# Kernel tuning notes

Hardware: AMD Instinct MI355X
Metric: run time of the kernel (lower is better)

The kernel has to match this reference:

```python
import jax, jax.numpy as jnp
import numpy as np

NUM_HEADS = 8
CHUNK = 2
TAU = 2.0

# --- LIF neuron with ATan surrogate gradient (spikingjelly MultiStepLIFNode, hard reset to 0, detach_reset) ---
@jax.custom_vjp
def spike(x):
    return (x >= 0.0).astype(x.dtype)

def _spike_fwd(x):
    return spike(x), x

def _spike_bwd(x, g):
    alpha = 2.0
    sg = (alpha / 2.0) / (1.0 + (jnp.pi / 2.0 * alpha * x) ** 2)
    return (g * sg,)

spike.defvjp(_spike_fwd, _spike_bwd)

def lif(x_seq, v_th=1.0):
    # x_seq: [T, ...]; v' = v + (x - v)/tau ; spike if v' >= v_th ; hard reset v=0 (reset path detached)
    def step(v, x):
        v = v + (x - v) / TAU
        s = spike(v - v_th)
        v = v * (1.0 - jax.lax.stop_gradient(s))
        return v, s
    _, s = jax.lax.scan(step, jnp.zeros_like(x_seq[0]), x_seq)
    return s

def conv1x1_bn(x, W, scale, bias, conv_bias=None):
    # 1x1 conv over channel dim + eval-mode BN (per-channel affine)
    y = jnp.einsum('tbchw,dc->tbdhw', x, W)
    if conv_bias is not None:
        y = y + conv_bias[None, None, :, None, None]
    return y * scale[None, None, :, None, None] + bias[None, None, :, None, None]


def setup_inputs() -> dict:
    key = jax.random.key(0)
    ks = jax.random.split(key, 16)
    T, B, C, H, W = 4, 32, 512, 16, 16
    s = 1.0 / np.sqrt(C)
    return {
        'x': jax.random.normal(ks[0], (T, B, C, H, W), jnp.float32),
        'Wq': jax.random.normal(ks[1], (C, C), jnp.float32) * s,
        'q_scale': jax.random.uniform(ks[2], (C,), jnp.float32, 0.5, 1.5),
        'q_bias': jax.random.normal(ks[3], (C,), jnp.float32) * 0.1,
        'Wk': jax.random.normal(ks[4], (C, C), jnp.float32) * s,
        'k_scale': jax.random.uniform(ks[5], (C,), jnp.float32, 0.5, 1.5),
        'k_bias': jax.random.normal(ks[6], (C,), jnp.float32) * 0.1,
        'Wv': jax.random.normal(ks[7], (C, C), jnp.float32) * s,
        'v_scale': jax.random.uniform(ks[8], (C,), jnp.float32, 0.5, 1.5),
        'v_bias': jax.random.normal(ks[9], (C,), jnp.float32) * 0.1,
        'Wp': jax.random.normal(ks[10], (C, C), jnp.float32) * s,
        'bp': jax.random.normal(ks[11], (C,), jnp.float32) * 0.1,
        'p_scale': jax.random.uniform(ks[12], (C,), jnp.float32, 0.5, 1.5),
        'p_bias': jax.random.normal(ks[13], (C,), jnp.float32) * 0.1,
    }


def reference(x, Wq, q_scale, q_bias, Wk, k_scale, k_bias, Wv, v_scale, v_bias, Wp, bp, p_scale, p_bias):
    T, B, C, H, W = x.shape
    N = H * W
    hd = C // NUM_HEADS
    identity = x

    xs = lif(x)  # shortcut_lif

    def qkv_branch(W_, sc, bi):
        y = lif(conv1x1_bn(xs, W_, sc, bi))           # [T,B,C,H,W] spikes
        # flatten(3).transpose(-1,-2).reshape(...heads...).permute == split C, swap N/hd
        return jnp.swapaxes(y.reshape(T, B, NUM_HEADS, hd, N), -1, -2)  # [T,B,h,N,hd]

    q = qkv_branch(Wq, q_scale, q_bias)
    k = qkv_branch(Wk, k_scale, k_bias)
    v = qkv_branch(Wv, v_scale, v_bias)

    # STAtten: temporal chunking, linear attention q @ (k^T v)
    scaling = 1.0 / H
    nc = T // CHUNK

    def to_chunks(y):  # [T,B,h,N,hd] -> [nc,B,h,CHUNK*N,hd]
        return (y.reshape(nc, CHUNK, B, NUM_HEADS, N, hd)
                 .transpose(0, 2, 3, 1, 4, 5)
                 .reshape(nc, B, NUM_HEADS, CHUNK * N, hd))

    qc, kc, vc = to_chunks(q), to_chunks(k), to_chunks(v)
    attn = jnp.einsum('nbhsd,nbhse->nbhde', kc, vc) * scaling   # [nc,B,h,hd,hd]
    out = jnp.einsum('nbhsd,nbhde->nbhse', qc, attn)            # [nc,B,h,CHUNK*N,hd]
    out = (out.reshape(nc, B, NUM_HEADS, CHUNK, N, hd)
              .transpose(0, 3, 1, 2, 4, 5)
              .reshape(T, B, NUM_HEADS, N, hd))

    x2 = jnp.swapaxes(out, -1, -2).reshape(T, B, C, N)          # [T,B,C,N]
    x2 = lif(x2, v_th=0.5).reshape(T, B, C, H, W)               # attn_lif

    x3 = conv1x1_bn(x2, Wp, p_scale, p_bias, conv_bias=bp)      # proj conv+BN
    return x3 + identity, v
```

## Files before the change

### kernel.cpp

```cpp
#include <hip/hip_runtime.h>

typedef unsigned short ushort_t;
typedef unsigned char u8;
typedef short bf16x8 __attribute__((ext_vector_type(8)));
typedef float f32x4 __attribute__((ext_vector_type(4)));

#define T_DIM 4
#define B_DIM 32
#define C_DIM 512
#define N_DIM 256

__device__ __forceinline__ float bf2f(ushort_t u) {
  union { unsigned int i; float f; } x;
  x.i = ((unsigned int)u) << 16;
  return x.f;
}
__device__ __forceinline__ ushort_t f2bf(float f) {
  unsigned int u = __float_as_uint(f);
  u = (u + 0x7FFFu + ((u >> 16) & 1u)) >> 16;
  return (ushort_t)u;
}

__device__ __forceinline__ void gload16(const void* g, void* l) {
  __builtin_amdgcn_global_load_lds(
      (const __attribute__((address_space(1))) unsigned int*)g,
      (__attribute__((address_space(3))) unsigned int*)l, 16, 0, 0);
}

__global__ __launch_bounds__(256) void k0_split(
    const float* __restrict__ Wq, const float* __restrict__ Wk,
    const float* __restrict__ Wv, const float* __restrict__ Wp,
    ushort_t* __restrict__ Sqkv, ushort_t* __restrict__ Sp)
{
  int gid = blockIdx.x * 256 + threadIdx.x;
  int w = gid >> 15;
  int off = (gid & 32767) * 8;
  const float* src = (w == 0) ? Wq : ((w == 1) ? Wk : ((w == 2) ? Wv : Wp));
  ushort_t* dst = (w < 3) ? (Sqkv + (size_t)w * 3 * 262144) : Sp;
  float wv[8];
  *(float4*)&wv[0] = *(const float4*)(src + off);
  *(float4*)&wv[4] = *(const float4*)(src + off + 4);
  ushort_t hi[8], mi[8], lo[8];
#pragma unroll
  for (int i = 0; i < 8; i++) {
    float f = wv[i];
    ushort_t h = f2bf(f);  float r  = f - bf2f(h);
    ushort_t m = f2bf(r);  float r2 = r - bf2f(m);
    ushort_t l = f2bf(r2);
    hi[i] = h; mi[i] = m; lo[i] = l;
  }
  *(uint4*)(dst + off)              = *(uint4*)&hi[0];
  *(uint4*)(dst + 262144 + off)     = *(uint4*)&mi[0];
  *(uint4*)(dst + 2 * 262144 + off) = *(uint4*)&lo[0];
}

__global__ __launch_bounds__(256) void k1_shortcut_lif(
    const float* __restrict__ x, u8* __restrict__ xsT8)
{
  const int n0 = blockIdx.x * 64;
  const int c0 = blockIdx.y * 64;
  const int b  = blockIdx.z;
  __shared__ u8 sm[64][80];
  const int tid = threadIdx.x;
  const int r  = tid >> 2;
  const int j0 = (tid & 3) * 16;
  float v[16];
#pragma unroll
  for (int i = 0; i < 16; i++) v[i] = 0.f;
  for (int t = 0; t < T_DIM; t++) {
    const float* xp = x + ((((size_t)t * B_DIM + b) * C_DIM) + c0 + r) * N_DIM + n0 + j0;
    float xv[16];
    *(float4*)&xv[0]  = *(const float4*)xp;
    *(float4*)&xv[4]  = *(const float4*)(xp + 4);
    *(float4*)&xv[8]  = *(const float4*)(xp + 8);
    *(float4*)&xv[12] = *(const float4*)(xp + 12);
    __syncthreads();
#pragma unroll
    for (int i = 0; i < 16; i++) {
      float nv = v[i] + (xv[i] - v[i]) * 0.5f;
      bool s = (nv >= 1.0f);
      v[i] = s ? 0.f : nv;
      sm[j0 + i][r] = s ? (u8)1 : (u8)0;
    }
    __syncthreads();
    union { uint4 u; u8 b[16]; } ov;
#pragma unroll
    for (int i = 0; i < 16; i++) ov.b[i] = sm[r][j0 + i];
    u8* op = xsT8 + ((((size_t)t * B_DIM + b) * N_DIM) + n0 + r) * C_DIM + c0 + j0;
    *(uint4*)op = ov.u;
  }
}

__global__ __launch_bounds__(512, 4) void k2_qkv(
    const u8* __restrict__ xsT8, const ushort_t* __restrict__ Sqkv,
    const float* __restrict__ qsc, const float* __restrict__ qbi,
    const float* __restrict__ ksc, const float* __restrict__ kbi,
    const float* __restrict__ vsc, const float* __restrict__ vbi,
    u8* __restrict__ qs8, u8* __restrict__ ks8, float* __restrict__ vout,
    u8* __restrict__ vs8)
{
  const int lin = blockIdx.x + blockIdx.y * 24;
  const int b   = (lin & 7) | (((lin >> 3) & 3) << 3);
  const int mt  = lin >> 5;
  const int branch = mt >> 3;
  const int mloc = (mt & 7) * 64;
  const ushort_t* Ws = Sqkv + (size_t)branch * 3 * 262144;
  const float* scp = (branch == 0) ? qsc : ((branch == 1) ? ksc : vsc);
  const float* bip = (branch == 0) ? qbi : ((branch == 1) ? kbi : vbi);

  __shared__ alignas(16) ushort_t As[4][2][64][32];
  __shared__ alignas(16) u8 Bs8[4][256][32];

  const int tid  = threadIdx.x;
  const int lane = tid & 63;
  const int wave = tid >> 6;
  const int wrow = (wave >> 1) * 16;
  const int wcol = (wave & 1) * 128;
  const int frow = lane & 15;
  const int fsl  = lane >> 4;

  const u8* Bb0 = xsT8 + (size_t)b * N_DIM * C_DIM;

  const int a0p = wave >> 2, a0q = wave & 3;
  const int arl = lane >> 2;
  const int acl = (((lane & 3) ^ ((arl >> 1) & 3)) * 8);
  const int brl = lane >> 1;
  const int bcl = (((lane & 1) ^ ((brl >> 2) & 1) ^ ((brl >> 3) & 1)) * 16);
  const int cbx = wave;

#define K2_STAGE(s_) {                                                                     \
    const int ss_ = (s_);                                                                  \
    const int t_ = ss_ >> 4; const int kb_ = (ss_ & 15) * 32; const int bf_ = ss_ & 3;     \
    gload16(Ws + (size_t)a0p * 262144 + (size_t)(mloc + a0q * 16 + arl) * 512 + kb_ + acl, \
            &As[bf_][a0p][a0q * 16][0]);                                                   \
    gload16(Bb0 + (size_t)t_ * (B_DIM * N_DIM * C_DIM) + (size_t)(cbx * 32 + brl) * 512 + kb_ + bcl, \
            &Bs8[bf_][cbx * 32][0]);                                                       \
  }

  f32x4 acc[8];
  float vst[32];
#pragma unroll
  for (int i = 0; i < 32; i++) vst[i] = 0.f;
#pragma unroll
  for (int j = 0; j < 8; j++) acc[j] = (f32x4){0.f, 0.f, 0.f, 0.f};

  const int crow0 = (lane >> 4) * 4;
  const int cn    = lane & 15;
  float sc4[4], bi4[4];
#pragma unroll
  for (int r = 0; r < 4; r++) {
    int c = mloc + wrow + crow0 + r;
    sc4[r] = scp[c]; bi4[r] = bip[c];
  }

  K2_STAGE(0);
  K2_STAGE(1);

  for (int s = 0; s < 64; s++) {
    const int cur = s & 3;
    if (s < 62) K2_STAGE(s + 2);

    if (s < 62)      asm volatile("s_waitcnt vmcnt(4)" ::: "memory");
    else if (s == 62) asm volatile("s_waitcnt vmcnt(2)" ::: "memory");
    else              asm volatile("s_waitcnt vmcnt(0)" ::: "memory");
    __builtin_amdgcn_s_barrier();
    __builtin_amdgcn_sched_barrier(0);

    bf16x8 af[2];
    const int ar = wrow + frow;
    const int asw = (fsl ^ ((ar >> 1) & 3)) * 8;
#pragma unroll
    for (int p = 0; p < 2; p++) af[p] = *(const bf16x8*)&As[cur][p][ar][asw];

#pragma unroll
    for (int j = 0; j < 8; j++) {
      const int row = wcol + j * 16 + frow;
      const int bx  = ((row >> 2) ^ (row >> 3)) & 1;
      const int bsw = (((fsl >> 1) ^ bx) << 4) + ((fsl & 1) << 3);
      uint2 raw = *(const uint2*)&Bs8[cur][row][bsw];
      union { bf16x8 v; unsigned int u[4]; } bu;
      bu.u[0] = __builtin_amdgcn_perm(0u, raw.x, 0x05010400u) * 0x3F80u;
      bu.u[1] = __builtin_amdgcn_perm(0u, raw.x, 0x07030602u) * 0x3F80u;
      bu.u[2] = __builtin_amdgcn_perm(0u, raw.y, 0x05010400u) * 0x3F80u;
      bu.u[3] = __builtin_amdgcn_perm(0u, raw.y, 0x07030602u) * 0x3F80u;
#pragma unroll
      for (int p = 0; p < 2; p++)
        acc[j] = __builtin_amdgcn_mfma_f32_16x16x32_bf16(af[p], bu.v, acc[j], 0, 0, 0);
    }

    if ((s & 15) == 15) {
      const int t = s >> 4;
      const size_t tb = (size_t)t * B_DIM + b;
      if (branch < 2) {
        u8* dst = (branch == 0) ? qs8 : ks8;
#pragma unroll
        for (int r = 0; r < 4; r++) {
          const int c = mloc + wrow + crow0 + r;
#pragma unroll
          for (int j = 0; j < 8; j++) {
            const int n = wcol + j * 16 + cn;
            float y = acc[j][r] * sc4[r] + bi4[r];
            const int vi = j * 4 + r;
            float v = vst[vi];
            v = v + (y - v) * 0.5f;
            bool sp = (v >= 1.0f);
            vst[vi] = sp ? 0.f : v;
            dst[(tb * C_DIM + c) * N_DIM + n] = sp ? (u8)1 : (u8)0;
          }
        }
      } else {
        const int hv = mloc >> 6;
        const int d0 = wrow + crow0;
#pragma unroll
        for (int j = 0; j < 8; j++) {
          const int n = wcol + j * 16 + cn;
          float ov[4];
          u8 sv[4];
#pragma unroll
          for (int r = 0; r < 4; r++) {
            float y = acc[j][r] * sc4[r] + bi4[r];
            const int vi = j * 4 + r;
            float v = vst[vi];
            v = v + (y - v) * 0.5f;
            bool sp = (v >= 1.0f);
            vst[vi] = sp ? 0.f : v;
            ov[r] = sp ? 1.0f : 0.0f;
            sv[r] = sp ? (u8)1 : (u8)0;
          }
          const size_t vbase = ((tb * 8 + hv) * N_DIM + n) * 64 + d0;
          *(float4*)(vout + vbase) = make_float4(ov[0], ov[1], ov[2], ov[3]);
          *(uchar4*)(vs8 + vbase)  = make_uchar4(sv[0], sv[1], sv[2], sv[3]);
        }
      }
#pragma unroll
      for (int j = 0; j < 8; j++) acc[j] = (f32x4){0.f, 0.f, 0.f, 0.f};
    }
  }
#undef K2_STAGE
}

__global__ __launch_bounds__(256) void k3_attn(
    const u8* __restrict__ ks8, const u8* __restrict__ vs8,
    float* __restrict__ attn)
{
  const int h  = blockIdx.x;
  const int b  = blockIdx.y;
  const int ch = blockIdx.z;
  __shared__ u8 KtT[64][80];
  __shared__ u8 Vt[64][80];
  const int tid = threadIdx.x;
  const int d0 = (tid >> 4) * 4;
  const int e0 = (tid & 15) * 4;
  float a[16];
#pragma unroll
  for (int i = 0; i < 16; i++) a[i] = 0.f;

  for (int tt = 0; tt < 2; tt++) {
    int t = ch * 2 + tt;
    for (int n0 = 0; n0 < 256; n0 += 64) {
      __syncthreads();
      {
        int d  = tid >> 2;
        int s0 = (tid & 3) * 16;
        union { uint4 u; u8 bvec[16]; } kb;
        kb.u = *(const uint4*)(ks8 + ((((size_t)t * B_DIM + b) * C_DIM) + h * 64 + d) * N_DIM + n0 + s0);
#pragma unroll
        for (int i = 0; i < 16; i++) KtT[s0 + i][d] = kb.bvec[i];
      }
      {
        const u8* vb = vs8 + ((((size_t)t * B_DIM + b) * 8 + h) * N_DIM + n0) * 64;
        int row = tid >> 2;
        int eo  = (tid & 3) * 16;
        *(uint4*)&Vt[row][eo] = *(const uint4*)(vb + (size_t)row * 64 + eo);
      }
      __syncthreads();
      for (int s = 0; s < 64; s++) {
        uchar4 kb = *(const uchar4*)&KtT[s][d0];
        float kv[4] = { (float)kb.x, (float)kb.y, (float)kb.z, (float)kb.w };
        uchar4 vr = *(const uchar4*)&Vt[s][e0];
        float vv[4] = { (float)vr.x, (float)vr.y, (float)vr.z, (float)vr.w };
#pragma unroll
        for (int i = 0; i < 4; i++)
#pragma unroll
          for (int j = 0; j < 4; j++) a[i * 4 + j] += kv[i] * vv[j];
      }
    }
  }
  float* ap = attn + ((((size_t)ch * B_DIM + b) * 8 + h) * 64 + d0) * 64 + e0;
#pragma unroll
  for (int i = 0; i < 4; i++)
#pragma unroll
    for (int j = 0; j < 4; j++)
      ap[i * 64 + j] = a[i * 4 + j] * 0.0625f;
}

__global__ __launch_bounds__(256) void k4_out_lif(
    const u8* __restrict__ qs8, const float* __restrict__ attn,
    u8* __restrict__ x2sT8)
{
  const int h  = blockIdx.x;
  const int b  = blockIdx.y;
  const int nc = blockIdx.z;
  __shared__ float At[64][68];
  __shared__ u8 Qt[64][80];
  const int tid = threadIdx.x;
  const int e0 = (tid >> 4) * 4;
  const int n0 = (tid & 15) * 4;
  float vst[16];
#pragma unroll
  for (int i = 0; i < 16; i++) vst[i] = 0.f;

  for (int t = 0; t < T_DIM; t++) {
    if ((t & 1) == 0) {
      __syncthreads();
      const float* ap = attn + ((((size_t)(t >> 1) * B_DIM + b) * 8) + h) * 4096;
      int dr = tid >> 2;
      int co = (tid & 3) * 16;
#pragma unroll
      for (int u = 0; u < 4; u++)
        *(float4*)&At[dr][co + u * 4] = *(const float4*)(ap + dr * 64 + co + u * 4);
    }
    __syncthreads();
    {
      int d  = tid >> 2;
      int so = (tid & 3) * 16;
      *(uint4*)&Qt[d][so] =
        *(const uint4*)(qs8 + ((((size_t)t * B_DIM + b) * C_DIM) + h * 64 + d) * N_DIM + nc * 64 + so);
    }
    __syncthreads();
    float acc[16];
#pragma unroll
    for (int i = 0; i < 16; i++) acc[i] = 0.f;
    for (int d = 0; d < 64; d++) {
      float4 av = *(const float4*)&At[d][e0];
      float avv[4] = { av.x, av.y, av.z, av.w };
      uchar4 qr = *(const uchar4*)&Qt[d][n0];
      float qv[4] = { (float)qr.x, (float)qr.y, (float)qr.z, (float)qr.w };
#pragma unroll
      for (int i = 0; i < 4; i++)
#pragma unroll
        for (int j = 0; j < 4; j++) acc[i * 4 + j] += avv[i] * qv[j];
    }
#pragma unroll
    for (int j = 0; j < 4; j++) {
      u8 sv[4];
#pragma unroll
      for (int i = 0; i < 4; i++) {
        int vi = i * 4 + j;
        float y = acc[i * 4 + j];
        float nv = vst[vi] + (y - vst[vi]) * 0.5f;
        bool s = (nv >= 0.5f);
        vst[vi] = s ? 0.f : nv;
        sv[i] = s ? (u8)1 : (u8)0;
      }
      int n = nc * 64 + n0 + j;
      u8* op = x2sT8 + ((((size_t)t * B_DIM + b) * N_DIM) + n) * C_DIM + h * 64 + e0;
      *(uchar4*)op = make_uchar4(sv[0], sv[1], sv[2], sv[3]);
    }
  }
}

__global__ __launch_bounds__(512, 4) void k5_proj(
    const u8* __restrict__ x2sT8, const ushort_t* __restrict__ Sp,
    const float* __restrict__ bp, const float* __restrict__ psc,
    const float* __restrict__ pbi,
    const float* __restrict__ x, float* __restrict__ out0)
{
  const int tb = blockIdx.x;
  const int mt = blockIdx.y;
  const int mloc = mt * 64;

  __shared__ alignas(16) ushort_t As[4][2][64][32];
  __shared__ alignas(16) u8 Bs8[4][256][32];

  const int tid  = threadIdx.x;
  const int lane = tid & 63;
  const int wave = tid >> 6;
  const int wrow = (wave >> 1) * 16;
  const int wcol = (wave & 1) * 128;
  const int frow = lane & 15;
  const int fsl  = lane >> 4;

  const u8* Bb = x2sT8 + (size_t)tb * N_DIM * C_DIM;

  const int a0p = wave >> 2, a0q = wave & 3;
  const int arl = lane >> 2;
  const int acl = (((lane & 3) ^ ((arl >> 1) & 3)) * 8);
  const int brl = lane >> 1;
  const int bcl = (((lane & 1) ^ ((brl >> 2) & 1) ^ ((brl >> 3) & 1)) * 16);
  const int cbx = wave;

#define K5_STAGE(s_) {                                                                     \
    const int ss_ = (s_); const int kb_ = ss_ * 32; const int bf_ = ss_ & 3;               \
    gload16(Sp + (size_t)a0p * 262144 + (size_t)(mloc + a0q * 16 + arl) * 512 + kb_ + acl, \
            &As[bf_][a0p][a0q * 16][0]);                                                   \
    gload16(Bb + (size_t)(cbx * 32 + brl) * 512 + kb_ + bcl, &Bs8[bf_][cbx * 32][0]);      \
  }

  f32x4 acc[8];
#pragma unroll
  for (int j = 0; j < 8; j++) acc[j] = (f32x4){0.f, 0.f, 0.f, 0.f};

  K5_STAGE(0);
  K5_STAGE(1);

  for (int s = 0; s < 16; s++) {
    const int cur = s & 3;
    if (s < 14) K5_STAGE(s + 2);

    if (s < 14)       asm volatile("s_waitcnt vmcnt(4)" ::: "memory");
    else if (s == 14) asm volatile("s_waitcnt vmcnt(2)" ::: "memory");
    else              asm volatile("s_waitcnt vmcnt(0)" ::: "memory");
    __builtin_amdgcn_s_barrier();
    __builtin_amdgcn_sched_barrier(0);

    bf16x8 af[2];
    const int ar = wrow + frow;
    const int asw = (fsl ^ ((ar >> 1) & 3)) * 8;
#pragma unroll
    for (int p = 0; p < 2; p++) af[p] = *(const bf16x8*)&As[cur][p][ar][asw];

#pragma unroll
    for (int j = 0; j < 8; j++) {
      const int row = wcol + j * 16 + frow;
      const int bx  = ((row >> 2) ^ (row >> 3)) & 1;
      const int bsw = (((fsl >> 1) ^ bx) << 4) + ((fsl & 1) << 3);
      uint2 raw = *(const uint2*)&Bs8[cur][row][bsw];
      union { bf16x8 v; unsigned int u[4]; } bu;
      bu.u[0] = __builtin_amdgcn_perm(0u, raw.x, 0x05010400u) * 0x3F80u;
      bu.u[1] = __builtin_amdgcn_perm(0u, raw.x, 0x07030602u) * 0x3F80u;
      bu.u[2] = __builtin_amdgcn_perm(0u, raw.y, 0x05010400u) * 0x3F80u;
      bu.u[3] = __builtin_amdgcn_perm(0u, raw.y, 0x07030602u) * 0x3F80u;
#pragma unroll
      for (int p = 0; p < 2; p++)
        acc[j] = __builtin_amdgcn_mfma_f32_16x16x32_bf16(af[p], bu.v, acc[j], 0, 0, 0);
    }
  }

  const int crow0 = (lane >> 4) * 4;
  const int cn    = lane & 15;
#pragma unroll
  for (int r = 0; r < 4; r++) {
    const int c = mloc + wrow + crow0 + r;
    const float scf = psc[c];
    const float bif = pbi[c];
    const float bpf = bp[c];
#pragma unroll
    for (int j = 0; j < 8; j++) {
      const int n = wcol + j * 16 + cn;
      const size_t idx = ((size_t)tb * C_DIM + c) * N_DIM + n;
      out0[idx] = (acc[j][r] + bpf) * scf + bif + x[idx];
    }
  }
#undef K5_STAGE
}

extern "C" void kernel_launch(void* const* d_in, const int* in_sizes, int n_in,
                              void* d_out, int out_size, void* d_ws, size_t ws_size,
                              hipStream_t stream) {
  const float* x   = (const float*)d_in[0];
  const float* Wq  = (const float*)d_in[1];
  const float* qsc = (const float*)d_in[2];
  const float* qbi = (const float*)d_in[3];
  const float* Wk  = (const float*)d_in[4];
  const float* ksc = (const float*)d_in[5];
  const float* kbi = (const float*)d_in[6];
  const float* Wv  = (const float*)d_in[7];
  const float* vsc = (const float*)d_in[8];
  const float* vbi = (const float*)d_in[9];
  const float* Wp  = (const float*)d_in[10];
  const float* bp  = (const float*)d_in[11];
  const float* psc = (const float*)d_in[12];
  const float* pbi = (const float*)d_in[13];

  float* out0 = (float*)d_out;
  float* out1 = out0 + 16777216;

  const size_t M16 = 16u * 1024u * 1024u;
  char* o0 = (char*)d_out;
  char* ws = (char*)d_ws;

  u8*       xsT8  = (u8*)(o0);
  u8*       qs8   = (u8*)(o0 + M16);
  u8*       ks8   = (u8*)(o0 + 2 * M16);
  ushort_t* Sqkv  = (ushort_t*)(o0 + 3 * M16);
  u8*       vs8   = (u8*)(o0 + 3 * M16 + 8u * 1024u * 1024u);
  float*    attn  = (float*)(o0);
  u8*       x2sT8 = (u8*)(ws);
  ushort_t* Sp    = (ushort_t*)(ws + M16);

  hipLaunchKernelGGL(k0_split,        dim3(512),        dim3(256), 0, stream,
                     Wq, Wk, Wv, Wp, Sqkv, Sp);
  hipLaunchKernelGGL(k1_shortcut_lif, dim3(4, 8, 32),   dim3(256), 0, stream, x, xsT8);
  hipLaunchKernelGGL(k2_qkv,          dim3(24, 32),     dim3(512), 0, stream,
                     xsT8, Sqkv, qsc, qbi, ksc, kbi, vsc, vbi, qs8, ks8, out1, vs8);
  hipLaunchKernelGGL(k3_attn,         dim3(8, 32, 2),   dim3(256), 0, stream, ks8, vs8, attn);
  hipLaunchKernelGGL(k4_out_lif,      dim3(8, 32, 4),   dim3(256), 0, stream, qs8, attn, x2sT8);
  hipLaunchKernelGGL(k5_proj,         dim3(128, 8),     dim3(512), 0, stream,
                     x2sT8, Sp, bp, psc, pbi, x, out0);
}
```

Measured before the change: 467.4 us.

## Move attention kernels to MFMA with transposed spike layouts and split-bf16 attn

Rewrites k3 (K^T V) and k4 (Q·attn + LIF) to use bf16 MFMA with async global-to-LDS staging, replacing scalar FMA loops. To feed the MFMAs, k2 now writes q and v spikes in transposed layouts. k3 stores attn as a hi/lo bf16 pair so precision stays close to fp32. Buffer placement also moves Sqkv into workspace. The k2 epilogue's v-spike stores become byte-scattered writes, which may cost some write efficiency.

```diff
diff --git a/kernel.cpp b/kernel.cpp
--- a/kernel.cpp
+++ b/kernel.cpp
@@ -25,6 +25,20 @@
   __builtin_amdgcn_global_load_lds(
       (const __attribute__((address_space(1))) unsigned int*)g,
       (__attribute__((address_space(3))) unsigned int*)l, 16, 0, 0);
+}
+
+__device__ __forceinline__ unsigned int spike2bf(unsigned int w) {
+  unsigned int r;
+  asm("v_mul_u32_u24 %0, 0x3f80, %1" : "=v"(r) : "v"(w));
+  return r;
+}
+__device__ __forceinline__ bf16x8 expand_spikes(uint2 raw) {
+  union { bf16x8 v; unsigned int u[4]; } bu;
+  bu.u[0] = spike2bf(__builtin_amdgcn_perm(0u, raw.x, 0x05010400u));
+  bu.u[1] = spike2bf(__builtin_amdgcn_perm(0u, raw.x, 0x07030602u));
+  bu.u[2] = spike2bf(__builtin_amdgcn_perm(0u, raw.y, 0x05010400u));
+  bu.u[3] = spike2bf(__builtin_amdgcn_perm(0u, raw.y, 0x07030602u));
+  return bu.v;
 }
 
 __global__ __launch_bounds__(256) void k0_split(
@@ -96,8 +110,8 @@
     const float* __restrict__ qsc, const float* __restrict__ qbi,
     const float* __restrict__ ksc, const float* __restrict__ kbi,
     const float* __restrict__ vsc, const float* __restrict__ vbi,
-    u8* __restrict__ qs8, u8* __restrict__ ks8, float* __restrict__ vout,
-    u8* __restrict__ vs8)
+    u8* __restrict__ qs8T, u8* __restrict__ ks8, float* __restrict__ vout,
+    u8* __restrict__ vs8T)
 {
   const int lin = blockIdx.x + blockIdx.y * 24;
   const int b   = (lin & 7) | (((lin >> 3) & 3) << 3);
@@ -160,7 +174,7 @@
     const int cur = s & 3;
     if (s < 62) K2_STAGE(s + 2);
 
-    if (s < 62)      asm volatile("s_waitcnt vmcnt(4)" ::: "memory");
+    if (s < 62)       asm volatile("s_waitcnt vmcnt(4)" ::: "memory");
     else if (s == 62) asm volatile("s_waitcnt vmcnt(2)" ::: "memory");
     else              asm volatile("s_waitcnt vmcnt(0)" ::: "memory");
     __builtin_amdgcn_s_barrier();
@@ -177,22 +191,34 @@
       const int row = wcol + j * 16 + frow;
       const int bx  = ((row >> 2) ^ (row >> 3)) & 1;
       const int bsw = (((fsl >> 1) ^ bx) << 4) + ((fsl & 1) << 3);
-      uint2 raw = *(const uint2*)&Bs8[cur][row][bsw];
-      union { bf16x8 v; unsigned int u[4]; } bu;
-      bu.u[0] = __builtin_amdgcn_perm(0u, raw.x, 0x05010400u) * 0x3F80u;
-      bu.u[1] = __builtin_amdgcn_perm(0u, raw.x, 0x07030602u) * 0x3F80u;
-      bu.u[2] = __builtin_amdgcn_perm(0u, raw.y, 0x05010400u) * 0x3F80u;
-      bu.u[3] = __builtin_amdgcn_perm(0u, raw.y, 0x07030602u) * 0x3F80u;
+      bf16x8 bv = expand_spikes(*(const uint2*)&Bs8[cur][row][bsw]);
 #pragma unroll
       for (int p = 0; p < 2; p++)
-        acc[j] = __builtin_amdgcn_mfma_f32_16x16x32_bf16(af[p], bu.v, acc[j], 0, 0, 0);
+        acc[j] = __builtin_amdgcn_mfma_f32_16x16x32_bf16(af[p], bv, acc[j], 0, 0, 0);
     }
 
     if ((s & 15) == 15) {
       const int t = s >> 4;
       const size_t tb = (size_t)t * B_DIM + b;
-      if (branch < 2) {
-        u8* dst = (branch == 0) ? qs8 : ks8;
+      if (branch == 0) {
+#pragma unroll
+        for (int j = 0; j < 8; j++) {
+          const int n = wcol + j * 16 + cn;
+          u8 sv[4];
+#pragma unroll
+          for (int r = 0; r < 4; r++) {
+            float y = acc[j][r] * sc4[r] + bi4[r];
+            const int vi = j * 4 + r;
+            float v = vst[vi];
+            v = v + (y - v) * 0.5f;
+            bool sp = (v >= 1.0f);
+            vst[vi] = sp ? 0.f : v;
+            sv[r] = sp ? (u8)1 : (u8)0;
+          }
+          *(uchar4*)(qs8T + (tb * N_DIM + n) * C_DIM + mloc + wrow + crow0) =
+              make_uchar4(sv[0], sv[1], sv[2], sv[3]);
+        }
+      } else if (branch == 1) {
 #pragma unroll
         for (int r = 0; r < 4; r++) {
           const int c = mloc + wrow + crow0 + r;
@@ -205,7 +231,7 @@
             v = v + (y - v) * 0.5f;
             bool sp = (v >= 1.0f);
             vst[vi] = sp ? 0.f : v;
-            dst[(tb * C_DIM + c) * N_DIM + n] = sp ? (u8)1 : (u8)0;
+            ks8[(tb * C_DIM + c) * N_DIM + n] = sp ? (u8)1 : (u8)0;
           }
         }
       } else {
@@ -227,9 +253,11 @@
             ov[r] = sp ? 1.0f : 0.0f;
             sv[r] = sp ? (u8)1 : (u8)0;
           }
-          const size_t vbase = ((tb * 8 + hv) * N_DIM + n) * 64 + d0;
-          *(float4*)(vout + vbase) = make_float4(ov[0], ov[1], ov[2], ov[3]);
-          *(uchar4*)(vs8 + vbase)  = make_uchar4(sv[0], sv[1], sv[2], sv[3]);
+          *(float4*)(vout + ((tb * 8 + hv) * N_DIM + n) * 64 + d0) =
+              make_float4(ov[0], ov[1], ov[2], ov[3]);
+#pragma unroll
+          for (int r = 0; r < 4; r++)
+            vs8T[((tb * 8 + hv) * 64 + d0 + r) * N_DIM + n] = sv[r];
         }
       }
 #pragma unroll
@@ -240,124 +268,192 @@
 }
 
 __global__ __launch_bounds__(256) void k3_attn(
-    const u8* __restrict__ ks8, const u8* __restrict__ vs8,
-    float* __restrict__ attn)
+    const u8* __restrict__ ks8, const u8* __restrict__ vs8T,
+    ushort_t* __restrict__ attnT2)
 {
   const int h  = blockIdx.x;
   const int b  = blockIdx.y;
   const int ch = blockIdx.z;
-  __shared__ u8 KtT[64][80];
-  __shared__ u8 Vt[64][80];
-  const int tid = threadIdx.x;
-  const int d0 = (tid >> 4) * 4;
-  const int e0 = (tid & 15) * 4;
-  float a[16];
-#pragma unroll
-  for (int i = 0; i < 16; i++) a[i] = 0.f;
-
-  for (int tt = 0; tt < 2; tt++) {
-    int t = ch * 2 + tt;
-    for (int n0 = 0; n0 < 256; n0 += 64) {
-      __syncthreads();
-      {
-        int d  = tid >> 2;
-        int s0 = (tid & 3) * 16;
-        union { uint4 u; u8 bvec[16]; } kb;
-        kb.u = *(const uint4*)(ks8 + ((((size_t)t * B_DIM + b) * C_DIM) + h * 64 + d) * N_DIM + n0 + s0);
-#pragma unroll
-        for (int i = 0; i < 16; i++) KtT[s0 + i][d] = kb.bvec[i];
-      }
-      {
-        const u8* vb = vs8 + ((((size_t)t * B_DIM + b) * 8 + h) * N_DIM + n0) * 64;
-        int row = tid >> 2;
-        int eo  = (tid & 3) * 16;
-        *(uint4*)&Vt[row][eo] = *(const uint4*)(vb + (size_t)row * 64 + eo);
-      }
-      __syncthreads();
-      for (int s = 0; s < 64; s++) {
-        uchar4 kb = *(const uchar4*)&KtT[s][d0];
-        float kv[4] = { (float)kb.x, (float)kb.y, (float)kb.z, (float)kb.w };
-        uchar4 vr = *(const uchar4*)&Vt[s][e0];
-        float vv[4] = { (float)vr.x, (float)vr.y, (float)vr.z, (float)vr.w };
-#pragma unroll
-        for (int i = 0; i < 4; i++)
-#pragma unroll
-          for (int j = 0; j < 4; j++) a[i * 4 + j] += kv[i] * vv[j];
-      }
-    }
-  }
-  float* ap = attn + ((((size_t)ch * B_DIM + b) * 8 + h) * 64 + d0) * 64 + e0;
-#pragma unroll
-  for (int i = 0; i < 4; i++)
-#pragma unroll
-    for (int j = 0; j < 4; j++)
-      ap[i * 64 + j] = a[i * 4 + j] * 0.0625f;
+  __shared__ alignas(16) u8 Ks[4][64][32];
+  __shared__ alignas(16) u8 Vs[4][64][32];
+  const int tid  = threadIdx.x;
+  const int lane = tid & 63;
+  const int wave = tid >> 6;
+  const int wrow = wave * 16;
+  const int frow = lane & 15;
+  const int fsl  = lane >> 4;
+  const int brl  = lane >> 1;
+  const int bcl  = (((lane & 1) ^ ((brl >> 2) & 1) ^ ((brl >> 3) & 1)) * 16);
+
+#define K3_STAGE(s_) {                                                                     \
+    const int ss_ = (s_);                                                                  \
+    const int t_ = ch * 2 + (ss_ >> 3); const int kb_ = (ss_ & 7) * 32; const int bf_ = ss_ & 3; \
+    if (wave < 2)                                                                          \
+      gload16(ks8 + ((((size_t)t_ * B_DIM + b) * C_DIM) + h * 64 + wave * 32 + brl) * N_DIM + kb_ + bcl, \
+              &Ks[bf_][wave * 32][0]);                                                     \
+    else                                                                                   \
+      gload16(vs8T + ((((size_t)t_ * B_DIM + b) * 8 + h) * 64 + (wave - 2) * 32 + brl) * N_DIM + kb_ + bcl, \
+              &Vs[bf_][(wave - 2) * 32][0]);                                               \
+  }
+
+  f32x4 acc[4];
+#pragma unroll
+  for (int i = 0; i < 4; i++) acc[i] = (f32x4){0.f, 0.f, 0.f, 0.f};
+
+  K3_STAGE(0);
+  K3_STAGE(1);
+
+  for (int s = 0; s < 16; s++) {
+    const int cur = s & 3;
+    if (s < 14) K3_STAGE(s + 2);
+
+    if (s < 14)       asm volatile("s_waitcnt vmcnt(2)" ::: "memory");
+    else if (s == 14) asm volatile("s_waitcnt vmcnt(1)" ::: "memory");
+    else              asm volatile("s_waitcnt vmcnt(0)" ::: "memory");
+    __builtin_amdgcn_s_barrier();
+    __builtin_amdgcn_sched_barrier(0);
+
+    const int arow = wrow + frow;
+    const int axx  = ((arow >> 2) ^ (arow >> 3)) & 1;
+    const int asw  = (((fsl >> 1) ^ axx) << 4) + ((fsl & 1) << 3);
+    bf16x8 af = expand_spikes(*(const uint2*)&Ks[cur][arow][asw]);
+
+#pragma unroll
+    for (int nt = 0; nt < 4; nt++) {
+      const int row = nt * 16 + frow;
+      const int bx  = ((row >> 2) ^ (row >> 3)) & 1;
+      const int bsw = (((fsl >> 1) ^ bx) << 4) + ((fsl & 1) << 3);
+      bf16x8 bv = expand_spikes(*(const uint2*)&Vs[cur][row][bsw]);
+      acc[nt] = __builtin_amdgcn_mfma_f32_16x16x32_bf16(af, bv, acc[nt], 0, 0, 0);
+    }
+  }
+
+  const int cn    = lane & 15;
+  const int crow0 = (lane >> 4) * 4;
+  const int d     = wrow + crow0;
+  const int ks2   = d >> 5;
+  const int dl    = d & 31;
+  const size_t blk = ((size_t)(ch * B_DIM + b) * 8 + h);
+#pragma unroll
+  for (int nt = 0; nt < 4; nt++) {
+    const int e = nt * 16 + cn;
+    union { ushort_t sv[4]; uint2 u; } H, M;
+#pragma unroll
+    for (int r = 0; r < 4; r++) {
+      float a = acc[nt][r] * 0.0625f;
+      ushort_t hi = f2bf(a);
+      float m = a - bf2f(hi);
+      H.sv[r] = hi;
+      M.sv[r] = f2bf(m);
+    }
+    *(uint2*)(attnT2 + ((blk * 2 + 0) * 2 + ks2) * 2048 + (size_t)e * 32 + dl) = H.u;
+    *(uint2*)(attnT2 + ((blk * 2 + 1) * 2 + ks2) * 2048 + (size_t)e * 32 + dl) = M.u;
+  }
+#undef K3_STAGE
 }
 
 __global__ __launch_bounds__(256) void k4_out_lif(
-    const u8* __restrict__ qs8, const float* __restrict__ attn,
+    const u8* __restrict__ qs8T, const ushort_t* __restrict__ attnT2,
     u8* __restrict__ x2sT8)
 {
   const int h  = blockIdx.x;
   const int b  = blockIdx.y;
   const int nc = blockIdx.z;
-  __shared__ float At[64][68];
-  __shared__ u8 Qt[64][80];
-  const int tid = threadIdx.x;
-  const int e0 = (tid >> 4) * 4;
-  const int n0 = (tid & 15) * 4;
-  float vst[16];
-#pragma unroll
-  for (int i = 0; i < 16; i++) vst[i] = 0.f;
-
-  for (int t = 0; t < T_DIM; t++) {
-    if ((t & 1) == 0) {
-      __syncthreads();
-      const float* ap = attn + ((((size_t)(t >> 1) * B_DIM + b) * 8) + h) * 4096;
-      int dr = tid >> 2;
-      int co = (tid & 3) * 16;
-#pragma unroll
-      for (int u = 0; u < 4; u++)
-        *(float4*)&At[dr][co + u * 4] = *(const float4*)(ap + dr * 64 + co + u * 4);
-    }
-    __syncthreads();
-    {
-      int d  = tid >> 2;
-      int so = (tid & 3) * 16;
-      *(uint4*)&Qt[d][so] =
-        *(const uint4*)(qs8 + ((((size_t)t * B_DIM + b) * C_DIM) + h * 64 + d) * N_DIM + nc * 64 + so);
-    }
-    __syncthreads();
-    float acc[16];
-#pragma unroll
-    for (int i = 0; i < 16; i++) acc[i] = 0.f;
-    for (int d = 0; d < 64; d++) {
-      float4 av = *(const float4*)&At[d][e0];
-      float avv[4] = { av.x, av.y, av.z, av.w };
-      uchar4 qr = *(const uchar4*)&Qt[d][n0];
-      float qv[4] = { (float)qr.x, (float)qr.y, (float)qr.z, (float)qr.w };
-#pragma unroll
-      for (int i = 0; i < 4; i++)
-#pragma unroll
-        for (int j = 0; j < 4; j++) acc[i * 4 + j] += avv[i] * qv[j];
-    }
-#pragma unroll
-    for (int j = 0; j < 4; j++) {
-      u8 sv[4];
-#pragma unroll
-      for (int i = 0; i < 4; i++) {
-        int vi = i * 4 + j;
-        float y = acc[i * 4 + j];
-        float nv = vst[vi] + (y - vst[vi]) * 0.5f;
-        bool s = (nv >= 0.5f);
-        vst[vi] = s ? 0.f : nv;
-        sv[i] = s ? (u8)1 : (u8)0;
+  __shared__ alignas(16) ushort_t As[2][2][2][64][32];
+  __shared__ alignas(16) u8 Bs[2][128][32];
+  const int tid  = threadIdx.x;
+  const int lane = tid & 63;
+  const int wave = tid >> 6;
+  const int wrow = wave * 16;
+  const int frow = lane & 15;
+  const int fsl  = lane >> 4;
+  const int arl  = lane >> 2;
+  const int acl  = (((lane & 3) ^ ((arl >> 1) & 3)) * 8);
+  const int brl  = lane >> 1;
+  const int bcl  = (((lane & 1) ^ ((brl >> 2) & 1) ^ ((brl >> 3) & 1)) * 16);
+
+#define K4_STAGEB(s_) {                                                                    \
+    const int ss_ = (s_); const int t_ = ss_ >> 1; const int ks_ = ss_ & 1;                \
+    gload16(qs8T + (((size_t)t_ * B_DIM + b) * N_DIM + nc * 128 + wave * 32 + brl) * C_DIM \
+                 + h * 64 + ks_ * 32 + bcl,                                                \
+            &Bs[ss_ & 1][wave * 32][0]);                                                   \
+  }
+
+#pragma unroll
+  for (int i = 0; i < 8; i++) {
+    const int c  = wave * 8 + i;
+    const int chb = c >> 4, c4 = c & 15;
+    const int p = c4 >> 3, ks = (c4 >> 2) & 1, g = c4 & 3;
+    const size_t blk = ((size_t)(chb * B_DIM + b) * 8 + h);
+    gload16(attnT2 + (((blk * 2 + p) * 2 + ks) * 64 + g * 16 + arl) * 32 + acl,
+            &As[chb][p][ks][g * 16][0]);
+  }
+  K4_STAGEB(0);
+  asm volatile("s_waitcnt vmcnt(0)" ::: "memory");
+  __builtin_amdgcn_s_barrier();
+  __builtin_amdgcn_sched_barrier(0);
+
+  f32x4 acc[8];
+  float vst[32];
+#pragma unroll
+  for (int i = 0; i < 32; i++) vst[i] = 0.f;
+
+  const int cn    = lane & 15;
+  const int crow0 = (lane >> 4) * 4;
+
+  for (int sg = 0; sg < 8; sg++) {
+    const int cur = sg & 1;
+    if (sg < 7) K4_STAGEB(sg + 1);
+
+    const int chb = sg >> 2, ks = sg & 1;
+    if (ks == 0) {
+#pragma unroll
+      for (int j = 0; j < 8; j++) acc[j] = (f32x4){0.f, 0.f, 0.f, 0.f};
+    }
+
+    bf16x8 af[2];
+    const int ar = wrow + frow;
+    const int asw = (fsl ^ ((ar >> 1) & 3)) * 8;
+#pragma unroll
+    for (int p = 0; p < 2; p++) af[p] = *(const bf16x8*)&As[chb][p][ks][ar][asw];
+
+#pragma unroll
+    for (int j = 0; j < 8; j++) {
+      const int row = j * 16 + frow;
+      const int bx  = ((row >> 2) ^ (row >> 3)) & 1;
+      const int bsw = (((fsl >> 1) ^ bx) << 4) + ((fsl & 1) << 3);
+      bf16x8 bv = expand_spikes(*(const uint2*)&Bs[cur][row][bsw]);
+#pragma unroll
+      for (int p = 0; p < 2; p++)
+        acc[j] = __builtin_amdgcn_mfma_f32_16x16x32_bf16(af[p], bv, acc[j], 0, 0, 0);
+    }
+
+    if (ks == 1) {
+      const int t = sg >> 1;
+      const size_t tb = (size_t)t * B_DIM + b;
+#pragma unroll
+      for (int j = 0; j < 8; j++) {
+        const int n = nc * 128 + j * 16 + cn;
+        u8 sv[4];
+#pragma unroll
+        for (int r = 0; r < 4; r++) {
+          const int vi = j * 4 + r;
+          float y = acc[j][r];
+          float nv = vst[vi] + (y - vst[vi]) * 0.5f;
+          bool sp = (nv >= 0.5f);
+          vst[vi] = sp ? 0.f : nv;
+          sv[r] = sp ? (u8)1 : (u8)0;
+        }
+        *(uchar4*)(x2sT8 + (tb * N_DIM + n) * C_DIM + h * 64 + wrow + crow0) =
+            make_uchar4(sv[0], sv[1], sv[2], sv[3]);
       }
-      int n = nc * 64 + n0 + j;
-      u8* op = x2sT8 + ((((size_t)t * B_DIM + b) * N_DIM) + n) * C_DIM + h * 64 + e0;
-      *(uchar4*)op = make_uchar4(sv[0], sv[1], sv[2], sv[3]);
-    }
-  }
+    }
+
+    asm volatile("s_waitcnt vmcnt(0)" ::: "memory");
+    __builtin_amdgcn_s_barrier();
+    __builtin_amdgcn_sched_barrier(0);
+  }
+#undef K4_STAGEB
 }
 
 __global__ __launch_bounds__(512, 4) void k5_proj(
@@ -425,15 +521,10 @@
       const int row = wcol + j * 16 + frow;
       const int bx  = ((row >> 2) ^ (row >> 3)) & 1;
       const int bsw = (((fsl >> 1) ^ bx) << 4) + ((fsl & 1) << 3);
-      uint2 raw = *(const uint2*)&Bs8[cur][row][bsw];
-      union { bf16x8 v; unsigned int u[4]; } bu;
-      bu.u[0] = __builtin_amdgcn_perm(0u, raw.x, 0x05010400u) * 0x3F80u;
-      bu.u[1] = __builtin_amdgcn_perm(0u, raw.x, 0x07030602u) * 0x3F80u;
-      bu.u[2] = __builtin_amdgcn_perm(0u, raw.y, 0x05010400u) * 0x3F80u;
-      bu.u[3] = __builtin_amdgcn_perm(0u, raw.y, 0x07030602u) * 0x3F80u;
+      bf16x8 bv = expand_spikes(*(const uint2*)&Bs8[cur][row][bsw]);
 #pragma unroll
       for (int p = 0; p < 2; p++)
-        acc[j] = __builtin_amdgcn_mfma_f32_16x16x32_bf16(af[p], bu.v, acc[j], 0, 0, 0);
+        acc[j] = __builtin_amdgcn_mfma_f32_16x16x32_bf16(af[p], bv, acc[j], 0, 0, 0);
     }
   }
 
@@ -480,22 +571,24 @@
   char* o0 = (char*)d_out;
   char* ws = (char*)d_ws;
 
-  u8*       xsT8  = (u8*)(o0);
-  u8*       qs8   = (u8*)(o0 + M16);
-  u8*       ks8   = (u8*)(o0 + 2 * M16);
-  ushort_t* Sqkv  = (ushort_t*)(o0 + 3 * M16);
-  u8*       vs8   = (u8*)(o0 + 3 * M16 + 8u * 1024u * 1024u);
-  float*    attn  = (float*)(o0);
-  u8*       x2sT8 = (u8*)(ws);
-  ushort_t* Sp    = (ushort_t*)(ws + M16);
+  u8*       xsT8   = (u8*)(o0);
+  ushort_t* attnT2 = (ushort_t*)(o0);
+  u8*       qs8T   = (u8*)(o0 + M16);
+  u8*       ks8    = (u8*)(o0 + 2 * M16);
+  u8*       vs8T   = (u8*)(o0 + 3 * M16);
+  u8*       x2sT8  = (u8*)(ws);
+  ushort_t* Sqkv   = (ushort_t*)(ws);
+  ushort_t* Sp     = (ushort_t*)(ws + M16);
 
   hipLaunchKernelGGL(k0_split,        dim3(512),        dim3(256), 0, stream,
                      Wq, Wk, Wv, Wp, Sqkv, Sp);
   hipLaunchKernelGGL(k1_shortcut_lif, dim3(4, 8, 32),   dim3(256), 0, stream, x, xsT8);
   hipLaunchKernelGGL(k2_qkv,          dim3(24, 32),     dim3(512), 0, stream,
-                     xsT8, Sqkv, qsc, qbi, ksc, kbi, vsc, vbi, qs8, ks8, out1, vs8);
-  hipLaunchKernelGGL(k3_attn,         dim3(8, 32, 2),   dim3(256), 0, stream, ks8, vs8, attn);
-  hipLaunchKernelGGL(k4_out_lif,      dim3(8, 32, 4),   dim3(256), 0, stream, qs8, attn, x2sT8);
+                     xsT8, Sqkv, qsc, qbi, ksc, kbi, vsc, vbi, qs8T, ks8, out1, vs8T);
+  hipLaunchKernelGGL(k3_attn,         dim3(8, 32, 2),   dim3(256), 0, stream,
+                     ks8, vs8T, attnT2);
+  hipLaunchKernelGGL(k4_out_lif,      dim3(8, 32, 2),   dim3(256), 0, stream,
+                     qs8T, attnT2, x2sT8);
   hipLaunchKernelGGL(k5_proj,         dim3(128, 8),     dim3(512), 0, stream,
                      x2sT8, Sp, bp, psc, pbi, x, out0);
 }
```

Result: faster. 430.1 us (-8.0%).
